# Kernel optimization log

Hardware: AMD Instinct MI355X
Metric: run time of the kernel (lower is better)

Reference implementation:

```python
import jax, jax.numpy as jnp
import numpy as np

B, S, D = 2, 2048, 1024
H = 16
HD = D // H

def setup_inputs() -> dict:
    key = jax.random.key(0)
    ks = jax.random.split(key, 9)
    scale = 1.0 / np.sqrt(D)
    return {
        "qi": jax.random.normal(ks[0], (B, S, D), jnp.float32),
        "ki": jax.random.normal(ks[1], (B, S, D), jnp.float32),
        "vi": jax.random.normal(ks[2], (B, S, D), jnp.float32),
        "Wq": jax.random.normal(ks[3], (D, D), jnp.float32) * scale,
        "Wq_def": jax.random.normal(ks[4], (D, D), jnp.float32) * scale,
        "Wk": jax.random.normal(ks[5], (D, D), jnp.float32) * scale,
        "Wk_def": jax.random.normal(ks[6], (D, D), jnp.float32) * scale,
        "Wv": jax.random.normal(ks[7], (D, D), jnp.float32) * scale,
        "Wo": jax.random.normal(ks[8], (D, D), jnp.float32) * scale,
    }

def _heads(x, W):
    # torch Linear: x @ W.T, then view (B,S,H,HD) and transpose -> (B,H,S,HD)
    return (x @ W.T).reshape(B, S, H, HD).transpose(0, 2, 1, 3)

def reference(qi, ki, vi, Wq, Wq_def, Wk, Wk_def, Wv, Wo):
    q = _heads(qi, Wq)
    q_def = _heads(qi, Wq_def)
    k = _heads(ki, Wk)
    k_def = _heads(ki, Wk_def)
    v = _heads(vi, Wv)
    inv_sqrt = 1.0 / jnp.sqrt(jnp.asarray(HD, qi.dtype))
    scores = jnp.einsum('bhse,bhte->bhst', q, k) * inv_sqrt
    def_scores = jnp.einsum('bhse,bhte->bhst', q_def, k_def) * inv_sqrt
    # defeasible weights: sigmoid(def_scores).sum over t -> [B,H,S], broadcast over query dim
    def_w = jax.nn.sigmoid(def_scores).sum(axis=3)  # [B,H,S]
    attn = jax.nn.softmax(scores * def_w[:, :, None, :], axis=-1)
    attended = jnp.einsum('bhst,bhtd->bshd', attn, v).reshape(B, S, D)
    return attended @ Wo.T
```

## Files before the change

### kernel.cpp

```cpp
#include <hip/hip_runtime.h>
#include <math.h>

#define BSZ 2
#define SEQ 2048
#define DIM 1024
#define NH 16
#define HDIM 64
#define MR (BSZ*SEQ)

typedef __attribute__((ext_vector_type(8))) short bf16x8;
typedef __attribute__((ext_vector_type(4))) short bf16x4;
typedef __attribute__((ext_vector_type(4))) float floatx4;

static __device__ __forceinline__ unsigned short f2bf(float x) {
    unsigned u = __float_as_uint(x);
    u += 0x7fffu + ((u >> 16) & 1u);
    return (unsigned short)(u >> 16);
}
static __device__ __forceinline__ float bf2f(unsigned short h) {
    return __uint_as_float(((unsigned)h) << 16);
}
#define MFMA16(a,b,c) __builtin_amdgcn_mfma_f32_16x16x32_bf16((a),(b),(c),0,0,0)

static __device__ __forceinline__ floatx4 pv_mfma(bf16x4 a, bf16x4 b, floatx4 c) {
#if __has_builtin(__builtin_amdgcn_mfma_f32_16x16x16bf16_1k)
    return __builtin_amdgcn_mfma_f32_16x16x16bf16_1k(a, b, c, 0, 0, 0);
#else
    bf16x8 a8 = {a[0],a[1],a[2],a[3],0,0,0,0};
    bf16x8 b8 = {b[0],b[1],b[2],b[3],0,0,0,0};
    return MFMA16(a8, b8, c);
#endif
}

__global__ __launch_bounds__(256)
void conv_split(const float* p0, const float* p1, const float* p2,
                const float* p3,
                unsigned short* o0, unsigned short* o1, unsigned short* o2,
                unsigned short* o3,
                int r0, int r1, int r2, int r3)
{
    const float* pin; unsigned short* pout; int rows;
    switch (blockIdx.y) {
        case 0: pin=p0; pout=o0; rows=r0; break;
        case 1: pin=p1; pout=o1; rows=r1; break;
        case 2: pin=p2; pout=o2; rows=r2; break;
        default: pin=p3; pout=o3; rows=r3; break;
    }
    size_t idx = (size_t)blockIdx.x * 256 + threadIdx.x;
    if (idx * 4 >= (size_t)rows * DIM) return;
    size_t row = (idx * 4) >> 10;
    int col = (int)((idx * 4) & 1023);
    float4 f = *(const float4*)(pin + idx * 4);
    ushort4 h, l;
    h.x = f2bf(f.x); l.x = f2bf(f.x - bf2f(h.x));
    h.y = f2bf(f.y); l.y = f2bf(f.y - bf2f(h.y));
    h.z = f2bf(f.z); l.z = f2bf(f.z - bf2f(h.z));
    h.w = f2bf(f.w); l.w = f2bf(f.w - bf2f(h.w));
    *(ushort4*)(pout + row * 2048 + col)        = h;
    *(ushort4*)(pout + row * 2048 + 1024 + col) = l;
}

__global__ __launch_bounds__(256)
void conv_hi(const float* p0, const float* p1, const float* p2,
             unsigned short* o0, unsigned short* o1, unsigned short* o2,
             int n0, int n1, int n2)
{
    const float* pin; unsigned short* pout; int n;
    switch (blockIdx.y) {
        case 0: pin=p0; pout=o0; n=n0; break;
        case 1: pin=p1; pout=o1; n=n1; break;
        default: pin=p2; pout=o2; n=n2; break;
    }
    size_t idx = (size_t)blockIdx.x * 256 + threadIdx.x;
    if (idx * 4 >= (size_t)n) return;
    float4 f = *(const float4*)(pin + idx * 4);
    ushort4 h;
    h.x = f2bf(f.x); h.y = f2bf(f.y); h.z = f2bf(f.z); h.w = f2bf(f.w);
    *(ushort4*)(pout + idx * 4) = h;
}

template<int EPI, bool SPLIT3>
__global__ __launch_bounds__(256)
void gemm_mfma(const unsigned short* __restrict__ A0, const unsigned short* __restrict__ A1,
               const unsigned short* __restrict__ B0, const unsigned short* __restrict__ B1,
               void* C0v, void* C1v, int lda, int ldb, int nkb)
{
    const unsigned short* A = blockIdx.z ? A1 : A0;
    const unsigned short* B = blockIdx.z ? B1 : B0;
    float* Cf = (float*)(blockIdx.z ? C1v : C0v);
    unsigned short* Cb = (unsigned short*)(blockIdx.z ? C1v : C0v);

    __shared__ __align__(16) unsigned short As[128][72];
    __shared__ __align__(16) unsigned short Bs[128][72];

    const int tid = threadIdx.x;
    const int lane = tid & 63, wv = tid >> 6;
    const int c = lane & 15, quad = lane >> 4;
    const int wm = wv >> 1, wn = wv & 1;
    const int rowBase = blockIdx.y << 7;
    const int colBase = blockIdx.x << 7;

    floatx4 acc[4][4];
#pragma unroll
    for (int i = 0; i < 4; ++i)
#pragma unroll
        for (int j = 0; j < 4; ++j) acc[i][j] = (floatx4){0.f,0.f,0.f,0.f};

    bf16x8 ar[4], br[4];
    {
#pragma unroll
        for (int i = 0; i < 4; ++i) {
            int f = tid + (i << 8);
            int r = f >> 3, kbk = (f & 7) << 3;
            ar[i] = *(const bf16x8*)(A + (size_t)(rowBase + r) * lda + kbk);
            br[i] = *(const bf16x8*)(B + (size_t)(colBase + r) * ldb + kbk);
        }
    }
    for (int kb = 0; kb < nkb; ++kb) {
        __syncthreads();
#pragma unroll
        for (int i = 0; i < 4; ++i) {
            int f = tid + (i << 8);
            int r = f >> 3, kbk = (f & 7) << 3;
            *(bf16x8*)&As[r][kbk] = ar[i];
            *(bf16x8*)&Bs[r][kbk] = br[i];
        }
        __syncthreads();
        if (kb + 1 < nkb) {
            int kn = kb + 1, aoff, boff;
            if (SPLIT3) {
                int t = kn >> 4, kk = (kn & 15) << 6;
                aoff = ((t == 1) ? 1024 : 0) + kk;
                boff = ((t == 2) ? 1024 : 0) + kk;
            } else { aoff = boff = kn << 6; }
#pragma unroll
            for (int i = 0; i < 4; ++i) {
                int f = tid + (i << 8);
                int r = f >> 3, kbk = (f & 7) << 3;
                ar[i] = *(const bf16x8*)(A + (size_t)(rowBase + r) * lda + aoff + kbk);
                br[i] = *(const bf16x8*)(B + (size_t)(colBase + r) * ldb + boff + kbk);
            }
        }
#pragma unroll
        for (int ks = 0; ks < 2; ++ks) {
            bf16x8 af[4], bfr[4];
#pragma unroll
            for (int i = 0; i < 4; ++i) {
                af[i]  = *(const bf16x8*)&As[wm*64 + i*16 + c][ks*32 + quad*8];
                bfr[i] = *(const bf16x8*)&Bs[wn*64 + i*16 + c][ks*32 + quad*8];
            }
#pragma unroll
            for (int mi = 0; mi < 4; ++mi)
#pragma unroll
                for (int ni = 0; ni < 4; ++ni)
                    acc[mi][ni] = MFMA16(af[mi], bfr[ni], acc[mi][ni]);
        }
    }
    const int row0 = rowBase + wm*64 + quad*4;
    if (EPI == 0) {
        const int col0 = colBase + wn*64 + c;
#pragma unroll
        for (int mi = 0; mi < 4; ++mi)
#pragma unroll
            for (int r = 0; r < 4; ++r) {
                size_t ro = (size_t)(row0 + mi*16 + r) * 1024 + col0;
#pragma unroll
                for (int ni = 0; ni < 4; ++ni)
                    Cf[ro + ni*16] = acc[mi][ni][r];
            }
    } else if (EPI == 1) {
        const int h = (colBase >> 6) + wn;
#pragma unroll
        for (int mi = 0; mi < 4; ++mi)
#pragma unroll
            for (int r = 0; r < 4; ++r) {
                int row = row0 + mi*16 + r;
                int b = row >> 11, s = row & 2047;
                size_t base = ((size_t)((b<<4) | h) * 2048 + s) * 128;
#pragma unroll
                for (int ni = 0; ni < 4; ++ni) {
                    int d = ni*16 + c;
                    float x = acc[mi][ni][r];
                    unsigned short hb = f2bf(x);
                    Cb[base + d]      = hb;
                    Cb[base + 64 + d] = f2bf(x - bf2f(hb));
                }
            }
    } else {
        const int h = (colBase >> 6) + wn;
#pragma unroll
        for (int mi = 0; mi < 4; ++mi) {
            int row = row0 + mi*16;
            int b = row >> 11, s = row & 2047;
#pragma unroll
            for (int ni = 0; ni < 4; ++ni) {
                int d = ni*16 + c;
                size_t base = ((size_t)((b<<4)|h) * 64 + d) * 2048 + s;
                ushort4 o4;
                o4.x = f2bf(acc[mi][ni][0]); o4.y = f2bf(acc[mi][ni][1]);
                o4.z = f2bf(acc[mi][ni][2]); o4.w = f2bf(acc[mi][ni][3]);
                *(ushort4*)(Cb + base) = o4;
            }
        }
    }
}

__global__ __launch_bounds__(256)
void defw_mfma(const unsigned short* __restrict__ qd,
               const unsigned short* __restrict__ kd,
               float* __restrict__ defw)
{
    __shared__ __align__(16) unsigned short Ks[64][136];
    const int tid = threadIdx.x;
    const int wv = tid >> 6, lane = tid & 63;
    const int c = lane & 15, quad = lane >> 4;
    const int bh = blockIdx.y;
    const int qbase = blockIdx.x << 7;
    const int trow = tid >> 2, seg = tid & 3;

    bf16x8 qhi[2][2], qlo[2][2];
#pragma unroll
    for (int mi = 0; mi < 2; ++mi) {
        const unsigned short* qrow =
            qd + ((size_t)bh*2048 + qbase + wv*32 + mi*16 + c)*128 + quad*8;
        qhi[mi][0] = *(const bf16x8*)(qrow);
        qhi[mi][1] = *(const bf16x8*)(qrow + 32);
        qlo[mi][0] = *(const bf16x8*)(qrow + 64);
        qlo[mi][1] = *(const bf16x8*)(qrow + 96);
    }
    float rs[2][4] = {{0.f,0.f,0.f,0.f},{0.f,0.f,0.f,0.f}};
    const unsigned short* kbase = kd + (size_t)bh*2048*128;
    bf16x8 kpre[4];
    {
        const unsigned short* kp = kbase + (size_t)trow*128 + seg*32;
#pragma unroll
        for (int u = 0; u < 4; ++u) kpre[u] = *(const bf16x8*)(kp + 8*u);
    }
    for (int kt = 0; kt < SEQ; kt += 64) {
        __syncthreads();
#pragma unroll
        for (int u = 0; u < 4; ++u) *(bf16x8*)&Ks[trow][seg*32 + 8*u] = kpre[u];
        __syncthreads();
        if (kt + 64 < SEQ) {
            const unsigned short* kp = kbase + (size_t)(kt + 64 + trow)*128 + seg*32;
#pragma unroll
            for (int u = 0; u < 4; ++u) kpre[u] = *(const bf16x8*)(kp + 8*u);
        }
#pragma unroll
        for (int nk = 0; nk < 4; ++nk) {
            const unsigned short* kr = &Ks[16*nk + c][quad*8];
            bf16x8 kh0 = *(const bf16x8*)(kr);
            bf16x8 kh1 = *(const bf16x8*)(kr + 32);
            bf16x8 kl0 = *(const bf16x8*)(kr + 64);
            bf16x8 kl1 = *(const bf16x8*)(kr + 96);
#pragma unroll
            for (int mi = 0; mi < 2; ++mi) {
                floatx4 s = {0.f,0.f,0.f,0.f};
                s = MFMA16(qhi[mi][0], kh0, s);
                s = MFMA16(qhi[mi][1], kh1, s);
                s = MFMA16(qlo[mi][0], kh0, s);
                s = MFMA16(qlo[mi][1], kh1, s);
                s = MFMA16(qhi[mi][0], kl0, s);
                s = MFMA16(qhi[mi][1], kl1, s);
#pragma unroll
                for (int r = 0; r < 4; ++r)
                    rs[mi][r] += 1.f / (1.f + __expf(-0.125f * s[r]));
            }
        }
    }
#pragma unroll
    for (int mi = 0; mi < 2; ++mi)
#pragma unroll
        for (int r = 0; r < 4; ++r) {
            float vv = rs[mi][r];
            vv += __shfl_xor(vv, 1, 16);
            vv += __shfl_xor(vv, 2, 16);
            vv += __shfl_xor(vv, 4, 16);
            vv += __shfl_xor(vv, 8, 16);
            if (c == 0)
                defw[(size_t)bh*SEQ + qbase + wv*32 + mi*16 + 4*quad + r]
                    = vv * 0.125f;
        }
}

__global__ __launch_bounds__(256)
void flash_mfma(const unsigned short* __restrict__ q,
                const unsigned short* __restrict__ kk,
                const unsigned short* __restrict__ vt,
                const float* __restrict__ dwg,
                unsigned short* __restrict__ o)
{
    __shared__ __align__(16) unsigned short Ks[64][136];
    __shared__ __align__(16) unsigned short Vs[64][72];
    const int tid = threadIdx.x;
    const int wv = tid >> 6, lane = tid & 63;
    const int c = lane & 15, quad = lane >> 4;
    const int bh = blockIdx.y, b = bh >> 4, h = bh & 15;
    const int qbase = blockIdx.x << 7;
    const int trow = tid >> 2, seg = tid & 3;

    bf16x8 qhi[2][2], qlo[2][2];
#pragma unroll
    for (int mi = 0; mi < 2; ++mi) {
        const unsigned short* qrow =
            q + ((size_t)bh*2048 + qbase + wv*32 + mi*16 + c)*128 + quad*8;
        qhi[mi][0] = *(const bf16x8*)(qrow);
        qhi[mi][1] = *(const bf16x8*)(qrow + 32);
        qlo[mi][0] = *(const bf16x8*)(qrow + 64);
        qlo[mi][1] = *(const bf16x8*)(qrow + 96);
    }
    floatx4 Oa[4][2];
#pragma unroll
    for (int nd = 0; nd < 4; ++nd)
#pragma unroll
        for (int mi = 0; mi < 2; ++mi) Oa[nd][mi] = (floatx4){0.f,0.f,0.f,0.f};
    float mrun[2] = {-3.0e38f, -3.0e38f}, lrun[2] = {0.f, 0.f};

    const unsigned short* kbase = kk + (size_t)bh*2048*128;
    const unsigned short* vbase = vt + (size_t)bh*64*2048;

    bf16x8 kpre[4], vpre[2];
    {
        const unsigned short* kp = kbase + (size_t)trow*128 + seg*32;
#pragma unroll
        for (int u = 0; u < 4; ++u) kpre[u] = *(const bf16x8*)(kp + 8*u);
        const unsigned short* vp = vbase + (size_t)trow*2048 + seg*16;
        vpre[0] = *(const bf16x8*)(vp);
        vpre[1] = *(const bf16x8*)(vp + 8);
    }

    for (int kt = 0; kt < SEQ; kt += 64) {
        __syncthreads();
#pragma unroll
        for (int u = 0; u < 4; ++u) *(bf16x8*)&Ks[trow][seg*32 + 8*u] = kpre[u];
        *(bf16x8*)&Vs[trow][seg*16 + 0] = vpre[0];
        *(bf16x8*)&Vs[trow][seg*16 + 8] = vpre[1];
        float dwf[4][4];
#pragma unroll
        for (int nk = 0; nk < 4; ++nk) {
            float4 d4 = *(const float4*)&dwg[(size_t)bh*SEQ + kt + nk*16 + quad*4];
            dwf[nk][0]=d4.x; dwf[nk][1]=d4.y; dwf[nk][2]=d4.z; dwf[nk][3]=d4.w;
        }
        __syncthreads();
        if (kt + 64 < SEQ) {
            const unsigned short* kp = kbase + (size_t)(kt + 64 + trow)*128 + seg*32;
#pragma unroll
            for (int u = 0; u < 4; ++u) kpre[u] = *(const bf16x8*)(kp + 8*u);
            const unsigned short* vp = vbase + (size_t)trow*2048 + (kt + 64) + seg*16;
            vpre[0] = *(const bf16x8*)(vp);
            vpre[1] = *(const bf16x8*)(vp + 8);
        }

        float z[2][4][4];
#pragma unroll
        for (int nk = 0; nk < 4; ++nk) {
            const unsigned short* kr = &Ks[16*nk + c][quad*8];
            bf16x8 kh0 = *(const bf16x8*)(kr);
            bf16x8 kh1 = *(const bf16x8*)(kr + 32);
            bf16x8 kl0 = *(const bf16x8*)(kr + 64);
            bf16x8 kl1 = *(const bf16x8*)(kr + 96);
#pragma unroll
            for (int mi = 0; mi < 2; ++mi) {
                floatx4 s = {0.f,0.f,0.f,0.f};
                s = MFMA16(kh0, qhi[mi][0], s);
                s = MFMA16(kh1, qhi[mi][1], s);
                s = MFMA16(kh0, qlo[mi][0], s);
                s = MFMA16(kh1, qlo[mi][1], s);
                s = MFMA16(kl0, qhi[mi][0], s);
                s = MFMA16(kl1, qhi[mi][1], s);
#pragma unroll
                for (int r = 0; r < 4; ++r) z[mi][nk][r] = s[r] * dwf[nk][r];
            }
        }
        float alpha[2];
#pragma unroll
        for (int mi = 0; mi < 2; ++mi) {
            float tm = z[mi][0][0];
#pragma unroll
            for (int nk = 0; nk < 4; ++nk)
#pragma unroll
                for (int r = 0; r < 4; ++r) tm = fmaxf(tm, z[mi][nk][r]);
            tm = fmaxf(tm, __shfl_xor(tm, 16));
            tm = fmaxf(tm, __shfl_xor(tm, 32));
            float mn = fmaxf(mrun[mi], tm);
            alpha[mi] = __expf(mrun[mi] - mn);
            mrun[mi] = mn;
            float rsum = 0.f;
#pragma unroll
            for (int nk = 0; nk < 4; ++nk)
#pragma unroll
                for (int r = 0; r < 4; ++r) {
                    z[mi][nk][r] = __expf(z[mi][nk][r] - mn);
                    rsum += z[mi][nk][r];
                }
            rsum += __shfl_xor(rsum, 16);
            rsum += __shfl_xor(rsum, 32);
            lrun[mi] = lrun[mi] * alpha[mi] + rsum;
        }
        bf16x4 pb[2][4];
#pragma unroll
        for (int mi = 0; mi < 2; ++mi)
#pragma unroll
            for (int nk = 0; nk < 4; ++nk) {
                bf16x4 p;
                p[0] = (short)f2bf(z[mi][nk][0]);
                p[1] = (short)f2bf(z[mi][nk][1]);
                p[2] = (short)f2bf(z[mi][nk][2]);
                p[3] = (short)f2bf(z[mi][nk][3]);
                pb[mi][nk] = p;
            }
#pragma unroll
        for (int nd = 0; nd < 4; ++nd)
#pragma unroll
            for (int mi = 0; mi < 2; ++mi)
#pragma unroll
                for (int r = 0; r < 4; ++r)
                    Oa[nd][mi][r] *= alpha[mi];
#pragma unroll
        for (int ks = 0; ks < 4; ++ks)
#pragma unroll
            for (int nd = 0; nd < 4; ++nd) {
                bf16x4 va = *(const bf16x4*)&Vs[nd*16 + c][ks*16 + quad*4];
#pragma unroll
                for (int mi = 0; mi < 2; ++mi)
                    Oa[nd][mi] = pv_mfma(va, pb[mi][ks], Oa[nd][mi]);
            }
    }
#pragma unroll
    for (int mi = 0; mi < 2; ++mi) {
        float invl = 1.f / lrun[mi];
        int s_abs = qbase + wv*32 + mi*16 + c;
        unsigned short* orow = o + ((size_t)(b*SEQ + s_abs))*DIM + h*HDIM;
#pragma unroll
        for (int nd = 0; nd < 4; ++nd) {
            ushort4 o4;
            o4.x = f2bf(Oa[nd][mi][0] * invl);
            o4.y = f2bf(Oa[nd][mi][1] * invl);
            o4.z = f2bf(Oa[nd][mi][2] * invl);
            o4.w = f2bf(Oa[nd][mi][3] * invl);
            *(ushort4*)(orow + nd*16 + quad*4) = o4;
        }
    }
}

extern "C" void kernel_launch(void* const* d_in, const int* in_sizes, int n_in,
                              void* d_out, int out_size, void* d_ws, size_t ws_size,
                              hipStream_t stream)
{
    (void)in_sizes; (void)n_in; (void)out_size; (void)ws_size;
    const float* qi     = (const float*)d_in[0];
    const float* ki     = (const float*)d_in[1];
    const float* vi     = (const float*)d_in[2];
    const float* Wq     = (const float*)d_in[3];
    const float* Wq_def = (const float*)d_in[4];
    const float* Wk     = (const float*)d_in[5];
    const float* Wk_def = (const float*)d_in[6];
    const float* Wv     = (const float*)d_in[7];
    const float* Wo     = (const float*)d_in[8];
    float* out = (float*)d_out;

    char* ws = (char*)d_ws;
    const size_t MB = 1024 * 1024;
    unsigned short* Aq  = (unsigned short*)(ws +  0*MB);
    unsigned short* Ak  = (unsigned short*)(ws + 16*MB);
    unsigned short* Bx  = (unsigned short*)(ws + 32*MB);
    unsigned short* By  = (unsigned short*)(ws + 36*MB);
    unsigned short* qs  = (unsigned short*)(ws + 40*MB);
    unsigned short* ks  = (unsigned short*)(ws + 56*MB);
    float*          dw  = (float*)(ws + 72*MB);
    unsigned short* Av  = (unsigned short*)(ws +  0*MB);
    unsigned short* Bv  = (unsigned short*)(ws +  8*MB);
    unsigned short* Bo  = (unsigned short*)(ws + 10*MB);
    unsigned short* Vt  = (unsigned short*)(ws + 12*MB);
    unsigned short* att = (unsigned short*)(ws + 20*MB);

    dim3 cb(256);
    dim3 gP(DIM/128, MR/128, 2);
    dim3 gS(DIM/128, MR/128, 1);
    dim3 gA(SEQ/128, BSZ*NH);

    conv_split<<<dim3(4096, 4), cb, 0, stream>>>(
        qi, ki, Wq_def, Wk_def, Aq, Ak, Bx, By, MR, MR, DIM, DIM);
    gemm_mfma<1, true><<<gP, cb, 0, stream>>>(Aq, Ak, Bx, By, qs, ks, 2048, 2048, 48);
    defw_mfma<<<gA, cb, 0, stream>>>(qs, ks, dw);
    conv_split<<<dim3(1024, 2), cb, 0, stream>>>(
        Wq, Wk, Wq, Wk, Bx, By, Bx, By, DIM, DIM, 0, 0);
    gemm_mfma<1, true><<<gP, cb, 0, stream>>>(Aq, Ak, Bx, By, qs, ks, 2048, 2048, 48);
    conv_hi<<<dim3(4096, 3), cb, 0, stream>>>(vi, Wv, Wo, Av, Bv, Bo,
                                              MR*DIM, DIM*DIM, DIM*DIM);
    gemm_mfma<2, false><<<gS, cb, 0, stream>>>(Av, Av, Bv, Bv, Vt, Vt, 1024, 1024, 16);
    flash_mfma<<<gA, cb, 0, stream>>>(qs, ks, Vt, dw, att);
    gemm_mfma<0, false><<<gS, cb, 0, stream>>>(att, att, Bo, Bo, out, out, 1024, 1024, 16);
}
```

Baseline: 482.9 us.

## Use direct global-to-LDS loads with XOR-swizzled shared tiles in GEMM

Replaces register-staged tile loading in the MFMA GEMM with global_load_lds direct copies into LDS, using an XOR swizzle on 16-byte chunks instead of row padding to avoid bank conflicts. This removes the register round trip and the separate LDS store instructions, and frees VGPRs. In exchange, the register prefetch of the next k-tile is dropped, so load latency is no longer overlapped with MFMA compute in the single-buffered loop.

```diff
diff --git a/kernel.cpp b/kernel.cpp
--- a/kernel.cpp
+++ b/kernel.cpp
@@ -30,6 +30,13 @@
     bf16x8 b8 = {b[0],b[1],b[2],b[3],0,0,0,0};
     return MFMA16(a8, b8, c);
 #endif
+}
+
+static __device__ __forceinline__ void gll16(const unsigned short* g, unsigned short* l) {
+    __builtin_amdgcn_global_load_lds(
+        (const __attribute__((address_space(1))) void*)g,
+        (__attribute__((address_space(3))) void*)l,
+        16, 0, 0);
 }
 
 __global__ __launch_bounds__(256)
@@ -90,8 +97,8 @@
     float* Cf = (float*)(blockIdx.z ? C1v : C0v);
     unsigned short* Cb = (unsigned short*)(blockIdx.z ? C1v : C0v);
 
-    __shared__ __align__(16) unsigned short As[128][72];
-    __shared__ __align__(16) unsigned short Bs[128][72];
+    __shared__ __align__(16) unsigned short As[128*64];
+    __shared__ __align__(16) unsigned short Bs[128*64];
 
     const int tid = threadIdx.x;
     const int lane = tid & 63, wv = tid >> 6;
@@ -100,54 +107,42 @@
     const int rowBase = blockIdx.y << 7;
     const int colBase = blockIdx.x << 7;
 
+    const int srow = lane >> 3;
+    const int schunk = (lane & 7) ^ srow;
+    const int segRow = wv * 32;
+    const unsigned short* Agb = A + (size_t)(rowBase + segRow + srow) * lda + schunk*8;
+    const unsigned short* Bgb = B + (size_t)(colBase + segRow + srow) * ldb + schunk*8;
+    unsigned short* Alb = &As[segRow * 64];
+    unsigned short* Blb = &Bs[segRow * 64];
+
     floatx4 acc[4][4];
 #pragma unroll
     for (int i = 0; i < 4; ++i)
 #pragma unroll
         for (int j = 0; j < 4; ++j) acc[i][j] = (floatx4){0.f,0.f,0.f,0.f};
 
-    bf16x8 ar[4], br[4];
-    {
+    for (int kb = 0; kb < nkb; ++kb) {
+        int aoff, boff;
+        if (SPLIT3) {
+            int t = kb >> 4, kk2 = (kb & 15) << 6;
+            aoff = ((t == 1) ? 1024 : 0) + kk2;
+            boff = ((t == 2) ? 1024 : 0) + kk2;
+        } else { aoff = boff = kb << 6; }
+        __syncthreads();
 #pragma unroll
         for (int i = 0; i < 4; ++i) {
-            int f = tid + (i << 8);
-            int r = f >> 3, kbk = (f & 7) << 3;
-            ar[i] = *(const bf16x8*)(A + (size_t)(rowBase + r) * lda + kbk);
-            br[i] = *(const bf16x8*)(B + (size_t)(colBase + r) * ldb + kbk);
-        }
-    }
-    for (int kb = 0; kb < nkb; ++kb) {
-        __syncthreads();
-#pragma unroll
-        for (int i = 0; i < 4; ++i) {
-            int f = tid + (i << 8);
-            int r = f >> 3, kbk = (f & 7) << 3;
-            *(bf16x8*)&As[r][kbk] = ar[i];
-            *(bf16x8*)&Bs[r][kbk] = br[i];
-        }
-        __syncthreads();
-        if (kb + 1 < nkb) {
-            int kn = kb + 1, aoff, boff;
-            if (SPLIT3) {
-                int t = kn >> 4, kk = (kn & 15) << 6;
-                aoff = ((t == 1) ? 1024 : 0) + kk;
-                boff = ((t == 2) ? 1024 : 0) + kk;
-            } else { aoff = boff = kn << 6; }
+            gll16(Agb + aoff + (size_t)(i*8)*lda, Alb + i*512);
+            gll16(Bgb + boff + (size_t)(i*8)*ldb, Blb + i*512);
+        }
+        __syncthreads();
+#pragma unroll
+        for (int ks = 0; ks < 2; ++ks) {
+            const int ch = ((ks << 2) + quad) ^ (c & 7);
+            bf16x8 af[4], bfr[4];
 #pragma unroll
             for (int i = 0; i < 4; ++i) {
-                int f = tid + (i << 8);
-                int r = f >> 3, kbk = (f & 7) << 3;
-                ar[i] = *(const bf16x8*)(A + (size_t)(rowBase + r) * lda + aoff + kbk);
-                br[i] = *(const bf16x8*)(B + (size_t)(colBase + r) * ldb + boff + kbk);
-            }
-        }
-#pragma unroll
-        for (int ks = 0; ks < 2; ++ks) {
-            bf16x8 af[4], bfr[4];
-#pragma unroll
-            for (int i = 0; i < 4; ++i) {
-                af[i]  = *(const bf16x8*)&As[wm*64 + i*16 + c][ks*32 + quad*8];
-                bfr[i] = *(const bf16x8*)&Bs[wn*64 + i*16 + c][ks*32 + quad*8];
+                af[i]  = *(const bf16x8*)&As[(wm*64 + i*16 + c)*64 + ch*8];
+                bfr[i] = *(const bf16x8*)&Bs[(wn*64 + i*16 + c)*64 + ch*8];
             }
 #pragma unroll
             for (int mi = 0; mi < 4; ++mi)
```

New measurement: 495.9 us. 1.03x slower.

## Compute defeasible branch in single fp16 instead of split-bf16 emulation

Applied to the files above, without the earlier changes.

The defeasible Q/K projections and the sigmoid-score kernel now use plain fp16 inputs with fp16 MFMA, replacing the three-term hi/lo bf16 split. This cuts the projection GEMM K-depth from 48 to 16 blocks, halves the defw K tile and Q/K storage, and drops four of six MFMAs per score tile. The main Q/K path keeps split-bf16 but now converts qi/ki once alongside Wq/Wk. The trade is lower precision in the defeasible weights, plus possible fp16 overflow or underflow in the inputs or products.

```diff
diff --git a/kernel.cpp b/kernel.cpp
--- a/kernel.cpp
+++ b/kernel.cpp
@@ -11,6 +11,7 @@
 typedef __attribute__((ext_vector_type(8))) short bf16x8;
 typedef __attribute__((ext_vector_type(4))) short bf16x4;
 typedef __attribute__((ext_vector_type(4))) float floatx4;
+typedef _Float16 f16x8 __attribute__((ext_vector_type(8)));
 
 static __device__ __forceinline__ unsigned short f2bf(float x) {
     unsigned u = __float_as_uint(x);
@@ -20,7 +21,18 @@
 static __device__ __forceinline__ float bf2f(unsigned short h) {
     return __uint_as_float(((unsigned)h) << 16);
 }
+static __device__ __forceinline__ unsigned short f2h(float x) {
+    union { _Float16 h; unsigned short u; } v;
+    v.h = (_Float16)x;
+    return v.u;
+}
 #define MFMA16(a,b,c) __builtin_amdgcn_mfma_f32_16x16x32_bf16((a),(b),(c),0,0,0)
+
+static __device__ __forceinline__ floatx4 mfma_f16(bf16x8 a, bf16x8 b, floatx4 c) {
+    union { bf16x8 s; f16x8 h; } ua, ub;
+    ua.s = a; ub.s = b;
+    return __builtin_amdgcn_mfma_f32_16x16x32_f16(ua.h, ub.h, c, 0, 0, 0);
+}
 
 static __device__ __forceinline__ floatx4 pv_mfma(bf16x4 a, bf16x4 b, floatx4 c) {
 #if __has_builtin(__builtin_amdgcn_mfma_f32_16x16x16bf16_1k)
@@ -61,6 +73,26 @@
 }
 
 __global__ __launch_bounds__(256)
+void conv_f16(const float* p0, const float* p1, const float* p2, const float* p3,
+              unsigned short* o0, unsigned short* o1, unsigned short* o2,
+              unsigned short* o3, int r0, int r1, int r2, int r3)
+{
+    const float* pin; unsigned short* pout; int rows;
+    switch (blockIdx.y) {
+        case 0: pin=p0; pout=o0; rows=r0; break;
+        case 1: pin=p1; pout=o1; rows=r1; break;
+        case 2: pin=p2; pout=o2; rows=r2; break;
+        default: pin=p3; pout=o3; rows=r3; break;
+    }
+    size_t idx = (size_t)blockIdx.x * 256 + threadIdx.x;
+    if (idx * 4 >= (size_t)rows * DIM) return;
+    float4 f = *(const float4*)(pin + idx * 4);
+    ushort4 h;
+    h.x = f2h(f.x); h.y = f2h(f.y); h.z = f2h(f.z); h.w = f2h(f.w);
+    *(ushort4*)(pout + idx * 4) = h;
+}
+
+__global__ __launch_bounds__(256)
 void conv_hi(const float* p0, const float* p1, const float* p2,
              unsigned short* o0, unsigned short* o1, unsigned short* o2,
              int n0, int n1, int n2)
@@ -79,7 +111,7 @@
     *(ushort4*)(pout + idx * 4) = h;
 }
 
-template<int EPI, bool SPLIT3>
+template<int EPI, bool SPLIT3, int DT>
 __global__ __launch_bounds__(256)
 void gemm_mfma(const unsigned short* __restrict__ A0, const unsigned short* __restrict__ A1,
                const unsigned short* __restrict__ B0, const unsigned short* __restrict__ B1,
@@ -152,8 +184,10 @@
 #pragma unroll
             for (int mi = 0; mi < 4; ++mi)
 #pragma unroll
-                for (int ni = 0; ni < 4; ++ni)
-                    acc[mi][ni] = MFMA16(af[mi], bfr[ni], acc[mi][ni]);
+                for (int ni = 0; ni < 4; ++ni) {
+                    if (DT == 0) acc[mi][ni] = MFMA16(af[mi], bfr[ni], acc[mi][ni]);
+                    else         acc[mi][ni] = mfma_f16(af[mi], bfr[ni], acc[mi][ni]);
+                }
         }
     }
     const int row0 = rowBase + wm*64 + quad*4;
@@ -186,7 +220,7 @@
                     Cb[base + 64 + d] = f2bf(x - bf2f(hb));
                 }
             }
-    } else {
+    } else if (EPI == 2) {
         const int h = (colBase >> 6) + wn;
 #pragma unroll
         for (int mi = 0; mi < 4; ++mi) {
@@ -202,6 +236,19 @@
                 *(ushort4*)(Cb + base) = o4;
             }
         }
+    } else {
+        const int h = (colBase >> 6) + wn;
+#pragma unroll
+        for (int mi = 0; mi < 4; ++mi)
+#pragma unroll
+            for (int r = 0; r < 4; ++r) {
+                int row = row0 + mi*16 + r;
+                int b = row >> 11, s = row & 2047;
+                size_t base = ((size_t)((b<<4) | h) * 2048 + s) * 64;
+#pragma unroll
+                for (int ni = 0; ni < 4; ++ni)
+                    Cb[base + ni*16 + c] = f2h(acc[mi][ni][r]);
+            }
     }
 }
 
@@ -210,7 +257,7 @@
                const unsigned short* __restrict__ kd,
                float* __restrict__ defw)
 {
-    __shared__ __align__(16) unsigned short Ks[64][136];
+    __shared__ __align__(16) unsigned short Ks[64][72];
     const int tid = threadIdx.x;
     const int wv = tid >> 6, lane = tid & 63;
     const int c = lane & 15, quad = lane >> 4;
@@ -218,50 +265,42 @@
     const int qbase = blockIdx.x << 7;
     const int trow = tid >> 2, seg = tid & 3;
 
-    bf16x8 qhi[2][2], qlo[2][2];
+    bf16x8 qf[2][2];
 #pragma unroll
     for (int mi = 0; mi < 2; ++mi) {
         const unsigned short* qrow =
-            qd + ((size_t)bh*2048 + qbase + wv*32 + mi*16 + c)*128 + quad*8;
-        qhi[mi][0] = *(const bf16x8*)(qrow);
-        qhi[mi][1] = *(const bf16x8*)(qrow + 32);
-        qlo[mi][0] = *(const bf16x8*)(qrow + 64);
-        qlo[mi][1] = *(const bf16x8*)(qrow + 96);
+            qd + ((size_t)bh*2048 + qbase + wv*32 + mi*16 + c)*64 + quad*8;
+        qf[mi][0] = *(const bf16x8*)(qrow);
+        qf[mi][1] = *(const bf16x8*)(qrow + 32);
     }
     float rs[2][4] = {{0.f,0.f,0.f,0.f},{0.f,0.f,0.f,0.f}};
-    const unsigned short* kbase = kd + (size_t)bh*2048*128;
-    bf16x8 kpre[4];
+    const unsigned short* kbase = kd + (size_t)bh*2048*64;
+    bf16x8 kpre[2];
     {
-        const unsigned short* kp = kbase + (size_t)trow*128 + seg*32;
-#pragma unroll
-        for (int u = 0; u < 4; ++u) kpre[u] = *(const bf16x8*)(kp + 8*u);
+        const unsigned short* kp = kbase + (size_t)trow*64 + seg*16;
+        kpre[0] = *(const bf16x8*)(kp);
+        kpre[1] = *(const bf16x8*)(kp + 8);
     }
     for (int kt = 0; kt < SEQ; kt += 64) {
         __syncthreads();
-#pragma unroll
-        for (int u = 0; u < 4; ++u) *(bf16x8*)&Ks[trow][seg*32 + 8*u] = kpre[u];
+        *(bf16x8*)&Ks[trow][seg*16 + 0] = kpre[0];
+        *(bf16x8*)&Ks[trow][seg*16 + 8] = kpre[1];
         __syncthreads();
         if (kt + 64 < SEQ) {
-            const unsigned short* kp = kbase + (size_t)(kt + 64 + trow)*128 + seg*32;
-#pragma unroll
-            for (int u = 0; u < 4; ++u) kpre[u] = *(const bf16x8*)(kp + 8*u);
+            const unsigned short* kp = kbase + (size_t)(kt + 64 + trow)*64 + seg*16;
+            kpre[0] = *(const bf16x8*)(kp);
+            kpre[1] = *(const bf16x8*)(kp + 8);
         }
 #pragma unroll
         for (int nk = 0; nk < 4; ++nk) {
             const unsigned short* kr = &Ks[16*nk + c][quad*8];
-            bf16x8 kh0 = *(const bf16x8*)(kr);
-            bf16x8 kh1 = *(const bf16x8*)(kr + 32);
-            bf16x8 kl0 = *(const bf16x8*)(kr + 64);
-            bf16x8 kl1 = *(const bf16x8*)(kr + 96);
+            bf16x8 k0 = *(const bf16x8*)(kr);
+            bf16x8 k1 = *(const bf16x8*)(kr + 32);
 #pragma unroll
             for (int mi = 0; mi < 2; ++mi) {
                 floatx4 s = {0.f,0.f,0.f,0.f};
-                s = MFMA16(qhi[mi][0], kh0, s);
-                s = MFMA16(qhi[mi][1], kh1, s);
-                s = MFMA16(qlo[mi][0], kh0, s);
-                s = MFMA16(qlo[mi][1], kh1, s);
-                s = MFMA16(qhi[mi][0], kl0, s);
-                s = MFMA16(qhi[mi][1], kl1, s);
+                s = mfma_f16(qf[mi][0], k0, s);
+                s = mfma_f16(qf[mi][1], k1, s);
 #pragma unroll
                 for (int r = 0; r < 4; ++r)
                     rs[mi][r] += 1.f / (1.f + __expf(-0.125f * s[r]));
@@ -461,10 +500,16 @@
 
     char* ws = (char*)d_ws;
     const size_t MB = 1024 * 1024;
+    unsigned short* Aqf  = (unsigned short*)(ws +  0*MB);
+    unsigned short* Akf  = (unsigned short*)(ws +  8*MB);
+    unsigned short* Bqdf = (unsigned short*)(ws + 16*MB);
+    unsigned short* Bkdf = (unsigned short*)(ws + 18*MB);
+    unsigned short* qdf  = (unsigned short*)(ws + 20*MB);
+    unsigned short* kdf  = (unsigned short*)(ws + 28*MB);
     unsigned short* Aq  = (unsigned short*)(ws +  0*MB);
     unsigned short* Ak  = (unsigned short*)(ws + 16*MB);
-    unsigned short* Bx  = (unsigned short*)(ws + 32*MB);
-    unsigned short* By  = (unsigned short*)(ws + 36*MB);
+    unsigned short* Bq  = (unsigned short*)(ws + 32*MB);
+    unsigned short* Bk  = (unsigned short*)(ws + 36*MB);
     unsigned short* qs  = (unsigned short*)(ws + 40*MB);
     unsigned short* ks  = (unsigned short*)(ws + 56*MB);
     float*          dw  = (float*)(ws + 72*MB);
@@ -479,16 +524,16 @@
     dim3 gS(DIM/128, MR/128, 1);
     dim3 gA(SEQ/128, BSZ*NH);
 
+    conv_f16<<<dim3(4096, 4), cb, 0, stream>>>(
+        qi, ki, Wq_def, Wk_def, Aqf, Akf, Bqdf, Bkdf, MR, MR, DIM, DIM);
+    gemm_mfma<3, false, 1><<<gP, cb, 0, stream>>>(Aqf, Akf, Bqdf, Bkdf, qdf, kdf, 1024, 1024, 16);
+    defw_mfma<<<gA, cb, 0, stream>>>(qdf, kdf, dw);
     conv_split<<<dim3(4096, 4), cb, 0, stream>>>(
-        qi, ki, Wq_def, Wk_def, Aq, Ak, Bx, By, MR, MR, DIM, DIM);
-    gemm_mfma<1, true><<<gP, cb, 0, stream>>>(Aq, Ak, Bx, By, qs, ks, 2048, 2048, 48);
-    defw_mfma<<<gA, cb, 0, stream>>>(qs, ks, dw);
-    conv_split<<<dim3(1024, 2), cb, 0, stream>>>(
-        Wq, Wk, Wq, Wk, Bx, By, Bx, By, DIM, DIM, 0, 0);
-    gemm_mfma<1, true><<<gP, cb, 0, stream>>>(Aq, Ak, Bx, By, qs, ks, 2048, 2048, 48);
+        qi, ki, Wq, Wk, Aq, Ak, Bq, Bk, MR, MR, DIM, DIM);
+    gemm_mfma<1, true, 0><<<gP, cb, 0, stream>>>(Aq, Ak, Bq, Bk, qs, ks, 2048, 2048, 48);
     conv_hi<<<dim3(4096, 3), cb, 0, stream>>>(vi, Wv, Wo, Av, Bv, Bo,
                                               MR*DIM, DIM*DIM, DIM*DIM);
-    gemm_mfma<2, false><<<gS, cb, 0, stream>>>(Av, Av, Bv, Bv, Vt, Vt, 1024, 1024, 16);
+    gemm_mfma<2, false, 0><<<gS, cb, 0, stream>>>(Av, Av, Bv, Bv, Vt, Vt, 1024, 1024, 16);
     flash_mfma<<<gA, cb, 0, stream>>>(qs, ks, Vt, dw, att);
-    gemm_mfma<0, false><<<gS, cb, 0, stream>>>(att, att, Bo, Bo, out, out, 1024, 1024, 16);
-}
+    gemm_mfma<0, false, 0><<<gS, cb, 0, stream>>>(att, att, Bo, Bo, out, out, 1024, 1024, 16);
+}
```

Result: faster. 442.3 us (-8.4%).
